# Kernel optimization log

Measured on AMD Instinct MI355X. Metric: run time of the kernel, lower is better.

## Reference

```python
import jax, jax.numpy as jnp
import numpy as np

HIDDEN = 600
INPUT_DIM = 300
BATCH = 64
SEQ = 512


def _lstm(x, W, U, b):
    """Keras-style LSTM, gate order (i, f, g, o). x: [B,T,D] -> [B,T,H]."""
    B, T, D = x.shape
    H = U.shape[0]
    xz = jnp.einsum('btd,dg->btg', x, W) + b  # precompute input projections [B,T,4H]

    def step(carry, xz_t):
        h, c = carry
        z = xz_t + h @ U  # [B,4H]
        i, f, g, o = jnp.split(z, 4, axis=-1)
        i = jax.nn.sigmoid(i)
        f = jax.nn.sigmoid(f)
        g = jnp.tanh(g)
        o = jax.nn.sigmoid(o)
        c = f * c + i * g
        h = o * jnp.tanh(c)
        return (h, c), h

    init = (jnp.zeros((B, H), x.dtype), jnp.zeros((B, H), x.dtype))
    _, hs = jax.lax.scan(step, init, jnp.swapaxes(xz, 0, 1))  # [T,B,H]
    return jnp.swapaxes(hs, 0, 1)


def _reverse_sequence(x, lengths):
    """tf.reverse_sequence along axis 1: reverse first lengths[b] steps, keep tail."""
    T = x.shape[1]
    t = jnp.arange(T)[None, :]
    L = lengths[:, None]
    idx = jnp.where(t < L, L - 1 - t, t)  # [B,T]
    return jnp.take_along_axis(x, idx[:, :, None], axis=1)


def setup_inputs() -> dict:
    key = jax.random.key(0)
    ks = jax.random.split(key, 8)
    inputs = jax.random.normal(ks[0], (BATCH, SEQ, INPUT_DIM), dtype=jnp.float32)
    lengths = jax.random.randint(ks[1], (BATCH,), 1, SEQ + 1, dtype=jnp.int32)
    s = 0.05
    Wf = jax.random.normal(ks[2], (INPUT_DIM, 4 * HIDDEN), dtype=jnp.float32) * s
    Uf = jax.random.normal(ks[3], (HIDDEN, 4 * HIDDEN), dtype=jnp.float32) * s
    bf = jnp.zeros((4 * HIDDEN,), dtype=jnp.float32)
    Wb = jax.random.normal(ks[4], (INPUT_DIM, 4 * HIDDEN), dtype=jnp.float32) * s
    Ub = jax.random.normal(ks[5], (HIDDEN, 4 * HIDDEN), dtype=jnp.float32) * s
    bb = jnp.zeros((4 * HIDDEN,), dtype=jnp.float32)
    return {"inputs": inputs, "lengths": lengths, "training": False,
            "Wf": Wf, "Uf": Uf, "bf": bf, "Wb": Wb, "Ub": Ub, "bb": bb}


def reference(inputs, lengths, training, Wf, Uf, bf, Wb, Ub, bb):
    # training=False -> Keras dropout is identity, so plain LSTMs are faithful.
    T = inputs.shape[1]
    seq_mask = (jnp.arange(T)[None, :] < lengths[:, None]).astype(inputs.dtype)  # [B,T]
    forward_outputs = _lstm(inputs, Wf, Uf, bf)
    reversed_inputs = _reverse_sequence(inputs, lengths)
    backward_outputs = _reverse_sequence(_lstm(reversed_inputs, Wb, Ub, bb), lengths)
    outputs = jnp.concatenate([forward_outputs, backward_outputs], axis=-1)  # [B,T,2H]
    outputs = outputs * seq_mask[:, :, None]
    # reduce_states=True: tf.reduce_mean over time divides by full T (not lengths)
    return jnp.mean(outputs, axis=1)
```

## Files before the change

kernel.cpp:

```cpp
#include <hip/hip_runtime.h>
#include <hip/hip_fp16.h>
#include <cmath>

typedef _Float16 f16;
typedef _Float16 half8 __attribute__((ext_vector_type(8)));
typedef float f32x4 __attribute__((ext_vector_type(4)));

#define P_WG   75
#define GRID_MAIN (2*P_WG)
#define G      12
#define RING   13

#define X16_ELEMS  (64u*512u*320u)
#define BPK_HALF   (2u*75u*2u*30u*64u*8u)
#define HBUF_F16   (2u*2u*64u*640u)
#define HBUF_WORDS (HBUF_F16/2u)
#define FLAG_WORDS 256u
#define E_OFF      96u

__global__ void lstm_prep(const float* __restrict__ x,
                          const float* __restrict__ Wf, const float* __restrict__ Uf,
                          const float* __restrict__ Wb, const float* __restrict__ Ub,
                          const int* __restrict__ len,
                          f16* __restrict__ x16h, f16* __restrict__ x16l,
                          f16* __restrict__ Bpk,
                          unsigned* __restrict__ hbw, unsigned* __restrict__ flags,
                          int* __restrict__ maxT, float* __restrict__ outp)
{
    const unsigned total = X16_ELEMS + BPK_HALF + HBUF_WORDS + FLAG_WORDS + 2u;
    for (unsigned e = blockIdx.x * blockDim.x + threadIdx.x; e < total;
         e += gridDim.x * blockDim.x) {
        if (e < X16_ELEMS) {
            unsigned k = e % 320u, r = e / 320u;
            float v = (k < 300u) ? x[r * 300u + k] : 0.0f;
            f16 hi = (f16)v;
            x16h[e] = hi;
            x16l[e] = (f16)((v - (float)hi) * 2048.0f);
        } else if (e < X16_ELEMS + BPK_HALF) {
            unsigned i = e - X16_ELEMS;
            unsigned j    = i & 7u,  r1 = i >> 3;
            unsigned lane = r1 & 63u, r2 = r1 >> 6;
            unsigned kt   = r2 % 30u, r3 = r2 / 30u;
            unsigned nt   = r3 & 1u,  r4 = r3 >> 1;
            unsigned p    = r4 % 75u, dw = r4 / 75u;
            unsigned k = kt * 32u + (lane >> 4) * 8u + j;
            unsigned n = nt * 16u + (lane & 15u);
            unsigned c = (n >> 3) * 600u + p * 8u + (n & 7u);
            float v = 0.0f;
            if (k < 300u)                    v = (dw ? Wb : Wf)[k * 2400u + c];
            else if (k >= 320u && k < 920u)  v = (dw ? Ub : Uf)[(k - 320u) * 2400u + c];
            f16 hi = (f16)v;
            unsigned base = (((((dw * 75u + p) * 2u + 0u) * 2u + nt) * 30u + kt) * 64u + lane) * 8u + j;
            Bpk[base]          = hi;
            Bpk[base + 30720u] = (f16)((v - (float)hi) * 2048.0f);
        } else if (e < X16_ELEMS + BPK_HALF + HBUF_WORDS) {
            hbw[e - X16_ELEMS - BPK_HALF] = 0u;
        } else if (e < X16_ELEMS + BPK_HALF + HBUF_WORDS + FLAG_WORDS) {
            unsigned q = e - (X16_ELEMS + BPK_HALF + HBUF_WORDS);
            unsigned q7 = q & 127u;
            flags[q] = (q7 < 75u || q7 == E_OFF) ? 0u : 0xFFFFFFFFu;
        } else {
            unsigned q = e - (X16_ELEMS + BPK_HALF + HBUF_WORDS + FLAG_WORDS);
            if (q == 0u) {
                int m = 1;
                for (int b = 0; b < 64; ++b) { int L = len[b]; m = (L > m) ? L : m; }
                *maxT = m;
            } else {
                outp[0] = 1000.0f;
            }
        }
    }
}

__global__ __launch_bounds__(256, 1)
void lstm_main(const f16* __restrict__ x16h, const f16* __restrict__ x16l,
               const f16* __restrict__ Bpk,
               f16* __restrict__ hbuf, float* __restrict__ xz,
               unsigned* flags, const int* __restrict__ maxT,
               const int* __restrict__ len,
               const float* __restrict__ bfv, const float* __restrict__ bbv,
               float* __restrict__ out)
{
    __shared__ f32x4 obox[4][4][2][64];
    __shared__ f16 hstage[64][8];
    __shared__ f16 Blds[4][10][512];

    const int tid  = threadIdx.x;
    const int wave = tid >> 6, lane = tid & 63;
    const int quad = lane >> 4, l15 = lane & 15;
    const int dir  = blockIdx.x & 1, p = blockIdx.x >> 1;
    const int pc   = p * 8;
    const int wg   = blockIdx.x;

    const int s0 = (wave < 2) ? 3 : 2;
    half8 Bh[5][2][2];
    const unsigned bpk_base = (unsigned)(dir * 75 + p) * 4u * 30u * 512u;
#pragma unroll
    for (int sp = 0; sp < 5; ++sp) {
        int kt = wave + 4 * (s0 + sp);
#pragma unroll
        for (int nt = 0; nt < 2; ++nt)
#pragma unroll
            for (int tm = 0; tm < 2; ++tm)
                Bh[sp][nt][tm] = *(const half8*)(Bpk +
                    (((((dir * 75 + p) * 2 + tm) * 2 + nt) * 30 + kt) * 64 + lane) * 8);
    }
    const float* bias = dir ? bbv : bfv;
    const float b0 = bias[((l15 >> 3)    ) * 600 + pc + (l15 & 7)];
    const float b1 = bias[((l15 >> 3) + 2) * 600 + pc + (l15 & 7)];

    int Lm[4], Lr[4];
#pragma unroll
    for (int mt = 0; mt < 4; ++mt) Lm[mt] = len[mt * 16 + l15];
    const int Lw = len[wave * 16 + l15];
#pragma unroll
    for (int r = 0; r < 4; ++r)   Lr[r]  = len[wave * 16 + quad * 4 + r];

    f16* hb0 = hbuf + dir * (2 * 64 * 640);
    unsigned* myflags = flags + dir * 128;
    float* myxz = xz + (size_t)wg * (RING * 64 * 32);
    float cst[4] = {0, 0, 0, 0}, sum[4] = {0, 0, 0, 0};
    const int T = *maxT;

    {
        f16* bl = &Blds[0][0][0];
#pragma unroll
        for (int blk = 0; blk < 4; ++blk)
            for (int i = tid; i < 640; i += 256)
                *(half8*)(bl + blk * 5120 + i * 8) =
                    *(const half8*)(Bpk + bpk_base + (unsigned)blk * 15360u + (unsigned)i * 8u);
    }
    __syncthreads();

#pragma unroll
    for (int jc = 0; jc < 3; ++jc) {
        int g = wave * 3 + jc;
        int tt = (g < 512) ? g : 511;
        unsigned arow[4];
#pragma unroll
        for (int mt = 0; mt < 4; ++mt) {
            int tx = tt;
            if (dir) tx = (tt < Lm[mt]) ? (Lm[mt] - 1 - tt) : tt;
            arow[mt] = ((unsigned)(mt * 16 + l15) * 512u + (unsigned)tx) * 320u + quad * 8;
        }
        f32x4 aH[4][2], aM[4][2];
#pragma unroll
        for (int mt = 0; mt < 4; ++mt)
#pragma unroll
            for (int nt = 0; nt < 2; ++nt) {
                aH[mt][nt] = f32x4{0.f, 0.f, 0.f, 0.f};
                aM[mt][nt] = f32x4{0.f, 0.f, 0.f, 0.f};
            }
#pragma unroll
        for (int kt = 0; kt < 10; ++kt) {
            const f16* bb = &Blds[0][0][0] + kt * 512 + lane * 8;
            half8 B00 = *(const half8*)(bb);
            half8 B01 = *(const half8*)(bb + 5120);
            half8 B10 = *(const half8*)(bb + 10240);
            half8 B11 = *(const half8*)(bb + 15360);
#pragma unroll
            for (int mt = 0; mt < 4; ++mt) {
                half8 Ah = *(const half8*)(x16h + arow[mt] + kt * 32);
                half8 Al = *(const half8*)(x16l + arow[mt] + kt * 32);
                aH[mt][0] = __builtin_amdgcn_mfma_f32_16x16x32_f16(Ah, B00, aH[mt][0], 0, 0, 0);
                aM[mt][0] = __builtin_amdgcn_mfma_f32_16x16x32_f16(Ah, B10, aM[mt][0], 0, 0, 0);
                aM[mt][0] = __builtin_amdgcn_mfma_f32_16x16x32_f16(Al, B00, aM[mt][0], 0, 0, 0);
                aH[mt][1] = __builtin_amdgcn_mfma_f32_16x16x32_f16(Ah, B01, aH[mt][1], 0, 0, 0);
                aM[mt][1] = __builtin_amdgcn_mfma_f32_16x16x32_f16(Ah, B11, aM[mt][1], 0, 0, 0);
                aM[mt][1] = __builtin_amdgcn_mfma_f32_16x16x32_f16(Al, B01, aM[mt][1], 0, 0, 0);
            }
        }
#pragma unroll
        for (int mt = 0; mt < 4; ++mt)
#pragma unroll
            for (int r = 0; r < 4; ++r) {
                unsigned rowi = (unsigned)(g * 64 + mt * 16 + quad * 4 + r) * 32u;
                myxz[rowi + l15]      = aH[mt][0][r] + aM[mt][0][r] * (1.0f / 2048.0f) + b0;
                myxz[rowi + 16 + l15] = aH[mt][1][r] + aM[mt][1][r] * (1.0f / 2048.0f) + b1;
            }
    }
    __syncthreads();

    for (int t = 0; t < T; ++t) {
        int tf = t + G;
        if (tf < T) {
            int tx = tf;
            if (dir) tx = (tf < Lw) ? (Lw - 1 - tf) : tf;
            unsigned arow = ((unsigned)(wave * 16 + l15) * 512u + (unsigned)tx) * 320u + quad * 8;
            f32x4 aH[2], aM[2];
            aH[0] = f32x4{0.f, 0.f, 0.f, 0.f}; aM[0] = f32x4{0.f, 0.f, 0.f, 0.f};
            aH[1] = f32x4{0.f, 0.f, 0.f, 0.f}; aM[1] = f32x4{0.f, 0.f, 0.f, 0.f};
#pragma unroll
            for (int kt = 0; kt < 10; ++kt) {
                const f16* bb = &Blds[0][0][0] + kt * 512 + lane * 8;
                half8 B00 = *(const half8*)(bb);
                half8 B01 = *(const half8*)(bb + 5120);
                half8 B10 = *(const half8*)(bb + 10240);
                half8 B11 = *(const half8*)(bb + 15360);
                half8 Ah = *(const half8*)(x16h + arow + kt * 32);
                half8 Al = *(const half8*)(x16l + arow + kt * 32);
                aH[0] = __builtin_amdgcn_mfma_f32_16x16x32_f16(Ah, B00, aH[0], 0, 0, 0);
                aM[0] = __builtin_amdgcn_mfma_f32_16x16x32_f16(Ah, B10, aM[0], 0, 0, 0);
                aM[0] = __builtin_amdgcn_mfma_f32_16x16x32_f16(Al, B00, aM[0], 0, 0, 0);
                aH[1] = __builtin_amdgcn_mfma_f32_16x16x32_f16(Ah, B01, aH[1], 0, 0, 0);
                aM[1] = __builtin_amdgcn_mfma_f32_16x16x32_f16(Ah, B11, aM[1], 0, 0, 0);
                aM[1] = __builtin_amdgcn_mfma_f32_16x16x32_f16(Al, B01, aM[1], 0, 0, 0);
            }
            int slot = tf % RING;
#pragma unroll
            for (int r = 0; r < 4; ++r) {
                unsigned rowi = (unsigned)(slot * 64 + wave * 16 + quad * 4 + r) * 32u;
                myxz[rowi + l15]      = aH[0][r] + aM[0][r] * (1.0f / 2048.0f) + b0;
                myxz[rowi + 16 + l15] = aH[1][r] + aM[1][r] * (1.0f / 2048.0f) + b1;
            }
        }

        float z0p[4], z1p[4];
        {
            int slot = t % RING;
            unsigned rbase = (unsigned)(slot * 64 + wave * 16 + quad * 4) * 32u;
#pragma unroll
            for (int r = 0; r < 4; ++r) {
                z0p[r] = myxz[rbase + r * 32 + l15];
                z1p[r] = myxz[rbase + r * 32 + 16 + l15];
            }
        }

        const f16* hcur = hb0 + (t & 1) * (64 * 640);
        f16*       hnxt = hb0 + ((t + 1) & 1) * (64 * 640);

        if (t > 0) {
            const unsigned tgt = (unsigned)t;
            if (wave == 0) {
                const unsigned long long* f8 = (const unsigned long long*)myflags;
                for (;;) {
                    unsigned long long v = ~0ull;
                    if (lane < 38)
                        v = __hip_atomic_load(&f8[lane], __ATOMIC_RELAXED, __HIP_MEMORY_SCOPE_AGENT);
                    bool bad = ((unsigned)v < tgt) || ((unsigned)(v >> 32) < tgt);
                    if (!__any(bad)) break;
                    __builtin_amdgcn_s_sleep(1);
                }
            }
            __syncthreads();
        }

        f32x4 accH[4][2], accM[4][2];
#pragma unroll
        for (int mt = 0; mt < 4; ++mt)
#pragma unroll
            for (int nt = 0; nt < 2; ++nt) {
                accH[mt][nt] = f32x4{0.f, 0.f, 0.f, 0.f};
                accM[mt][nt] = f32x4{0.f, 0.f, 0.f, 0.f};
            }

        unsigned long long pre[3][8];
        const f16* hq = hcur + quad * 8;
#define HLOAD(W, SP)                                                                     \
        { const int kt_ = wave + 4 * (s0 + (SP));                                        \
          const f16* hp_ = hq + (kt_ * 32 - 320);                                        \
          _Pragma("unroll")                                                              \
          for (int mt_ = 0; mt_ < 4; ++mt_) {                                            \
              const unsigned long long* q_ =                                             \
                  (const unsigned long long*)(hp_ + (unsigned)(mt_ * 16 + l15) * 640u);  \
              pre[W][mt_ * 2]     = __hip_atomic_load(q_,     __ATOMIC_RELAXED,          \
                                                      __HIP_MEMORY_SCOPE_AGENT);         \
              pre[W][mt_ * 2 + 1] = __hip_atomic_load(q_ + 1, __ATOMIC_RELAXED,          \
                                                      __HIP_MEMORY_SCOPE_AGENT);         \
          } }

        HLOAD(0, 0)
        HLOAD(1, 1)
        HLOAD(2, 2)
#pragma unroll
        for (int sp = 0; sp < 5; ++sp) {
#pragma unroll
            for (int mt = 0; mt < 4; ++mt) {
                union { unsigned long long u[2]; half8 h; } xu;
                xu.u[0] = pre[sp % 3][mt * 2];
                xu.u[1] = pre[sp % 3][mt * 2 + 1];
                half8 Ah = xu.h;
                accH[mt][0] = __builtin_amdgcn_mfma_f32_16x16x32_f16(Ah, Bh[sp][0][0], accH[mt][0], 0, 0, 0);
                accM[mt][0] = __builtin_amdgcn_mfma_f32_16x16x32_f16(Ah, Bh[sp][0][1], accM[mt][0], 0, 0, 0);
                accH[mt][1] = __builtin_amdgcn_mfma_f32_16x16x32_f16(Ah, Bh[sp][1][0], accH[mt][1], 0, 0, 0);
                accM[mt][1] = __builtin_amdgcn_mfma_f32_16x16x32_f16(Ah, Bh[sp][1][1], accM[mt][1], 0, 0, 0);
            }
            if (sp == 0) HLOAD(0, 3)
            if (sp == 1) HLOAD(1, 4)
        }
#undef HLOAD

        __syncthreads();
#pragma unroll
        for (int mt = 0; mt < 4; ++mt)
#pragma unroll
            for (int nt = 0; nt < 2; ++nt)
                obox[wave][mt][nt][lane] = accH[mt][nt] + accM[mt][nt] * (1.0f / 2048.0f);
        __syncthreads();
        f32x4 z0 = obox[0][wave][0][lane] + obox[1][wave][0][lane]
                 + obox[2][wave][0][lane] + obox[3][wave][0][lane];
        f32x4 z1 = obox[0][wave][1][lane] + obox[1][wave][1][lane]
                 + obox[2][wave][1][lane] + obox[3][wave][1][lane];
        z0 += f32x4{z0p[0], z0p[1], z0p[2], z0p[3]};
        z1 += f32x4{z1p[0], z1p[1], z1p[2], z1p[3]};

#pragma unroll
        for (int r = 0; r < 4; ++r) {
            float zi = z0[r], zg = z1[r];
            float zf = __shfl_xor(z0[r], 8, 64);
            float zo = __shfl_xor(z1[r], 8, 64);
            if (l15 < 8) {
                float ig = 1.0f / (1.0f + __expf(-zi));
                float fg = 1.0f / (1.0f + __expf(-zf));
                float gg = tanhf(zg);
                float og = 1.0f / (1.0f + __expf(-zo));
                float c  = fg * cst[r] + ig * gg;
                cst[r] = c;
                float h = og * tanhf(c);
                if (t < Lr[r]) sum[r] += h;
                hstage[wave * 16 + quad * 4 + r][l15] = (f16)h;
            }
        }
        __syncthreads();
        if (tid < 128) {
            int rr = tid >> 1, hf = tid & 1;
            unsigned long long v = *(const unsigned long long*)&hstage[rr][hf * 4];
            __hip_atomic_store(
                (unsigned long long*)(hnxt + (unsigned)rr * 640u + pc + hf * 4),
                v, __ATOMIC_RELAXED, __HIP_MEMORY_SCOPE_AGENT);
        }
        __syncthreads();
        if (tid == 0)
            __hip_atomic_store(myflags + p, (unsigned)(t + 1),
                               __ATOMIC_RELAXED, __HIP_MEMORY_SCOPE_AGENT);
    }

    if (l15 < 8) {
#pragma unroll
        for (int r = 0; r < 4; ++r)
            out[(wave * 16 + quad * 4 + r) * 1200 + dir * 600 + pc + l15] =
                sum[r] * (1.0f / 512.0f);
    }
}

extern "C" void kernel_launch(void* const* d_in, const int* in_sizes, int n_in,
                              void* d_out, int out_size, void* d_ws, size_t ws_size,
                              hipStream_t stream) {
    const float* x   = (const float*)d_in[0];
    const int*   len = (const int*)  d_in[1];
    const float* Wf  = (const float*)d_in[3];
    const float* Uf  = (const float*)d_in[4];
    const float* bfv = (const float*)d_in[5];
    const float* Wb  = (const float*)d_in[6];
    const float* Ub  = (const float*)d_in[7];
    const float* bbv = (const float*)d_in[8];
    float* outp = (float*)d_out;

    char* w = (char*)d_ws;
    f16*      x16hp = (f16*)w;
    f16*      x16lp = (f16*)(w + 20971520);
    f16*      bpkp  = (f16*)(w + 41943040);
    f16*      hbufp = (f16*)(w + 60375040);
    float*    xzp   = (float*)(w + 60702720);
    unsigned* flagp = (unsigned*)(w + 76677120);
    int*      maxtp = (int*)(w + 76678144);

    hipLaunchKernelGGL(lstm_prep, dim3(1024), dim3(256), 0, stream,
                       x, Wf, Uf, Wb, Ub, len,
                       x16hp, x16lp, bpkp, (unsigned*)hbufp, flagp, maxtp, outp);

    hipLaunchKernelGGL(lstm_main, dim3(GRID_MAIN), dim3(256), 0, stream,
                       x16hp, x16lp, bpkp, hbufp, xzp, flagp, maxtp, len, bfv, bbv, outp);
}
```

Baseline: 4.954 ms.

## Interleave forward and backward directions within each workgroup, halving grid

The grid shrinks from 150 to 75 workgroups, and each workgroup now processes both LSTM directions in alternation at every timestep. Recurrent weights are reloaded from global memory per step instead of staying resident in registers. Both directions' input-projection tiles are kept in LDS. The likely intent is to overlap one direction's flag wait and latency with the other's compute, at the cost of serialising both directions on one CU. It also adds per-step weight reload traffic and doubles LDS use.

Result: slower. 9.751 ms (+96.9%).

```diff
diff --git a/kernel.cpp b/kernel.cpp
--- a/kernel.cpp
+++ b/kernel.cpp
@@ -7,7 +7,7 @@
 typedef float f32x4 __attribute__((ext_vector_type(4)));
 
 #define P_WG   75
-#define GRID_MAIN (2*P_WG)
+#define GRID_MAIN P_WG
 #define G      12
 #define RING   13
 
@@ -58,7 +58,7 @@
         } else if (e < X16_ELEMS + BPK_HALF + HBUF_WORDS + FLAG_WORDS) {
             unsigned q = e - (X16_ELEMS + BPK_HALF + HBUF_WORDS);
             unsigned q7 = q & 127u;
-            flags[q] = (q7 < 75u || q7 == E_OFF) ? 0u : 0xFFFFFFFFu;
+            flags[q] = (q7 < 75u) ? 0u : 0xFFFFFFFFu;
         } else {
             unsigned q = e - (X16_ELEMS + BPK_HALF + HBUF_WORDS + FLAG_WORDS);
             if (q == 0u) {
@@ -83,31 +83,29 @@
 {
     __shared__ f32x4 obox[4][4][2][64];
     __shared__ f16 hstage[64][8];
-    __shared__ f16 Blds[4][10][512];
+    __shared__ f16 Blds[2][4][10][512];
 
     const int tid  = threadIdx.x;
     const int wave = tid >> 6, lane = tid & 63;
     const int quad = lane >> 4, l15 = lane & 15;
-    const int dir  = blockIdx.x & 1, p = blockIdx.x >> 1;
+    const int p    = blockIdx.x;
     const int pc   = p * 8;
-    const int wg   = blockIdx.x;
 
     const int s0 = (wave < 2) ? 3 : 2;
-    half8 Bh[5][2][2];
-    const unsigned bpk_base = (unsigned)(dir * 75 + p) * 4u * 30u * 512u;
-#pragma unroll
-    for (int sp = 0; sp < 5; ++sp) {
-        int kt = wave + 4 * (s0 + sp);
-#pragma unroll
-        for (int nt = 0; nt < 2; ++nt)
-#pragma unroll
-            for (int tm = 0; tm < 2; ++tm)
-                Bh[sp][nt][tm] = *(const half8*)(Bpk +
-                    (((((dir * 75 + p) * 2 + tm) * 2 + nt) * 30 + kt) * 64 + lane) * 8);
-    }
-    const float* bias = dir ? bbv : bfv;
-    const float b0 = bias[((l15 >> 3)    ) * 600 + pc + (l15 & 7)];
-    const float b1 = bias[((l15 >> 3) + 2) * 600 + pc + (l15 & 7)];
+
+    const unsigned bb_base[2] = { (unsigned)(0 * 75 + p) * 4u * 30u * 512u,
+                                  (unsigned)(1 * 75 + p) * 4u * 30u * 512u };
+    f16* hb[2]      = { hbuf, hbuf + (2 * 64 * 640) };
+    unsigned* fl[2] = { flags, flags + 128 };
+    float* mx[2]    = { xz + (size_t)(p * 2 + 0) * (RING * 64 * 32),
+                        xz + (size_t)(p * 2 + 1) * (RING * 64 * 32) };
+    float b0a[2], b1a[2];
+    {
+        const int c0 = ((l15 >> 3)) * 600 + pc + (l15 & 7);
+        const int c1 = ((l15 >> 3) + 2) * 600 + pc + (l15 & 7);
+        b0a[0] = bfv[c0]; b1a[0] = bfv[c1];
+        b0a[1] = bbv[c0]; b1a[1] = bbv[c1];
+    }
 
     int Lm[4], Lr[4];
 #pragma unroll
@@ -116,231 +114,250 @@
 #pragma unroll
     for (int r = 0; r < 4; ++r)   Lr[r]  = len[wave * 16 + quad * 4 + r];
 
-    f16* hb0 = hbuf + dir * (2 * 64 * 640);
-    unsigned* myflags = flags + dir * 128;
-    float* myxz = xz + (size_t)wg * (RING * 64 * 32);
-    float cst[4] = {0, 0, 0, 0}, sum[4] = {0, 0, 0, 0};
+    float cst[2][4] = {{0,0,0,0},{0,0,0,0}}, sum[2][4] = {{0,0,0,0},{0,0,0,0}};
     const int T = *maxT;
 
-    {
-        f16* bl = &Blds[0][0][0];
+#pragma unroll
+    for (int dd = 0; dd < 2; ++dd) {
+        f16* bl = &Blds[dd][0][0][0];
 #pragma unroll
         for (int blk = 0; blk < 4; ++blk)
             for (int i = tid; i < 640; i += 256)
                 *(half8*)(bl + blk * 5120 + i * 8) =
-                    *(const half8*)(Bpk + bpk_base + (unsigned)blk * 15360u + (unsigned)i * 8u);
+                    *(const half8*)(Bpk + bb_base[dd] + (unsigned)blk * 15360u + (unsigned)i * 8u);
     }
     __syncthreads();
 
 #pragma unroll
-    for (int jc = 0; jc < 3; ++jc) {
-        int g = wave * 3 + jc;
-        int tt = (g < 512) ? g : 511;
-        unsigned arow[4];
-#pragma unroll
-        for (int mt = 0; mt < 4; ++mt) {
-            int tx = tt;
-            if (dir) tx = (tt < Lm[mt]) ? (Lm[mt] - 1 - tt) : tt;
-            arow[mt] = ((unsigned)(mt * 16 + l15) * 512u + (unsigned)tx) * 320u + quad * 8;
-        }
-        f32x4 aH[4][2], aM[4][2];
-#pragma unroll
-        for (int mt = 0; mt < 4; ++mt)
-#pragma unroll
-            for (int nt = 0; nt < 2; ++nt) {
-                aH[mt][nt] = f32x4{0.f, 0.f, 0.f, 0.f};
-                aM[mt][nt] = f32x4{0.f, 0.f, 0.f, 0.f};
-            }
-#pragma unroll
-        for (int kt = 0; kt < 10; ++kt) {
-            const f16* bb = &Blds[0][0][0] + kt * 512 + lane * 8;
-            half8 B00 = *(const half8*)(bb);
-            half8 B01 = *(const half8*)(bb + 5120);
-            half8 B10 = *(const half8*)(bb + 10240);
-            half8 B11 = *(const half8*)(bb + 15360);
+    for (int dd = 0; dd < 2; ++dd) {
+#pragma unroll
+        for (int jc = 0; jc < 3; ++jc) {
+            int g = wave * 3 + jc;
+            int tt = (g < 512) ? g : 511;
+            unsigned arow[4];
 #pragma unroll
             for (int mt = 0; mt < 4; ++mt) {
-                half8 Ah = *(const half8*)(x16h + arow[mt] + kt * 32);
-                half8 Al = *(const half8*)(x16l + arow[mt] + kt * 32);
-                aH[mt][0] = __builtin_amdgcn_mfma_f32_16x16x32_f16(Ah, B00, aH[mt][0], 0, 0, 0);
-                aM[mt][0] = __builtin_amdgcn_mfma_f32_16x16x32_f16(Ah, B10, aM[mt][0], 0, 0, 0);
-                aM[mt][0] = __builtin_amdgcn_mfma_f32_16x16x32_f16(Al, B00, aM[mt][0], 0, 0, 0);
-                aH[mt][1] = __builtin_amdgcn_mfma_f32_16x16x32_f16(Ah, B01, aH[mt][1], 0, 0, 0);
-                aM[mt][1] = __builtin_amdgcn_mfma_f32_16x16x32_f16(Ah, B11, aM[mt][1], 0, 0, 0);
-                aM[mt][1] = __builtin_amdgcn_mfma_f32_16x16x32_f16(Al, B01, aM[mt][1], 0, 0, 0);
-            }
-        }
-#pragma unroll
-        for (int mt = 0; mt < 4; ++mt)
-#pragma unroll
-            for (int r = 0; r < 4; ++r) {
-                unsigned rowi = (unsigned)(g * 64 + mt * 16 + quad * 4 + r) * 32u;
-                myxz[rowi + l15]      = aH[mt][0][r] + aM[mt][0][r] * (1.0f / 2048.0f) + b0;
-                myxz[rowi + 16 + l15] = aH[mt][1][r] + aM[mt][1][r] * (1.0f / 2048.0f) + b1;
-            }
-    }
-    __syncthreads();
-
-    for (int t = 0; t < T; ++t) {
-        int tf = t + G;
-        if (tf < T) {
-            int tx = tf;
-            if (dir) tx = (tf < Lw) ? (Lw - 1 - tf) : tf;
-            unsigned arow = ((unsigned)(wave * 16 + l15) * 512u + (unsigned)tx) * 320u + quad * 8;
-            f32x4 aH[2], aM[2];
-            aH[0] = f32x4{0.f, 0.f, 0.f, 0.f}; aM[0] = f32x4{0.f, 0.f, 0.f, 0.f};
-            aH[1] = f32x4{0.f, 0.f, 0.f, 0.f}; aM[1] = f32x4{0.f, 0.f, 0.f, 0.f};
+                int tx = tt;
+                if (dd) tx = (tt < Lm[mt]) ? (Lm[mt] - 1 - tt) : tt;
+                arow[mt] = ((unsigned)(mt * 16 + l15) * 512u + (unsigned)tx) * 320u + quad * 8;
+            }
+            f32x4 aH[4][2], aM[4][2];
+#pragma unroll
+            for (int mt = 0; mt < 4; ++mt)
+#pragma unroll
+                for (int nt = 0; nt < 2; ++nt) {
+                    aH[mt][nt] = f32x4{0.f, 0.f, 0.f, 0.f};
+                    aM[mt][nt] = f32x4{0.f, 0.f, 0.f, 0.f};
+                }
 #pragma unroll
             for (int kt = 0; kt < 10; ++kt) {
-                const f16* bb = &Blds[0][0][0] + kt * 512 + lane * 8;
+                const f16* bb = &Blds[dd][0][0][0] + kt * 512 + lane * 8;
                 half8 B00 = *(const half8*)(bb);
                 half8 B01 = *(const half8*)(bb + 5120);
                 half8 B10 = *(const half8*)(bb + 10240);
                 half8 B11 = *(const half8*)(bb + 15360);
-                half8 Ah = *(const half8*)(x16h + arow + kt * 32);
-                half8 Al = *(const half8*)(x16l + arow + kt * 32);
-                aH[0] = __builtin_amdgcn_mfma_f32_16x16x32_f16(Ah, B00, aH[0], 0, 0, 0);
-                aM[0] = __builtin_amdgcn_mfma_f32_16x16x32_f16(Ah, B10, aM[0], 0, 0, 0);
-                aM[0] = __builtin_amdgcn_mfma_f32_16x16x32_f16(Al, B00, aM[0], 0, 0, 0);
-                aH[1] = __builtin_amdgcn_mfma_f32_16x16x32_f16(Ah, B01, aH[1], 0, 0, 0);
-                aM[1] = __builtin_amdgcn_mfma_f32_16x16x32_f16(Ah, B11, aM[1], 0, 0, 0);
-                aM[1] = __builtin_amdgcn_mfma_f32_16x16x32_f16(Al, B01, aM[1], 0, 0, 0);
-            }
-            int slot = tf % RING;
+#pragma unroll
+                for (int mt = 0; mt < 4; ++mt) {
+                    half8 Ah = *(const half8*)(x16h + arow[mt] + kt * 32);
+                    half8 Al = *(const half8*)(x16l + arow[mt] + kt * 32);
+                    aH[mt][0] = __builtin_amdgcn_mfma_f32_16x16x32_f16(Ah, B00, aH[mt][0], 0, 0, 0);
+                    aM[mt][0] = __builtin_amdgcn_mfma_f32_16x16x32_f16(Ah, B10, aM[mt][0], 0, 0, 0);
+                    aM[mt][0] = __builtin_amdgcn_mfma_f32_16x16x32_f16(Al, B00, aM[mt][0], 0, 0, 0);
+                    aH[mt][1] = __builtin_amdgcn_mfma_f32_16x16x32_f16(Ah, B01, aH[mt][1], 0, 0, 0);
+                    aM[mt][1] = __builtin_amdgcn_mfma_f32_16x16x32_f16(Ah, B11, aM[mt][1], 0, 0, 0);
+                    aM[mt][1] = __builtin_amdgcn_mfma_f32_16x16x32_f16(Al, B01, aM[mt][1], 0, 0, 0);
+                }
+            }
+#pragma unroll
+            for (int mt = 0; mt < 4; ++mt)
+#pragma unroll
+                for (int r = 0; r < 4; ++r) {
+                    unsigned rowi = (unsigned)(g * 64 + mt * 16 + quad * 4 + r) * 32u;
+                    mx[dd][rowi + l15]      = aH[mt][0][r] + aM[mt][0][r] * (1.0f / 2048.0f) + b0a[dd];
+                    mx[dd][rowi + 16 + l15] = aH[mt][1][r] + aM[mt][1][r] * (1.0f / 2048.0f) + b1a[dd];
+                }
+        }
+    }
+    __syncthreads();
+
+    for (int t = 0; t < T; ++t) {
+#pragma unroll
+        for (int dd = 0; dd < 2; ++dd) {
+            half8 Bh[5][2][2];
+#pragma unroll
+            for (int sp = 0; sp < 5; ++sp) {
+                int kt = wave + 4 * (s0 + sp);
+#pragma unroll
+                for (int nt = 0; nt < 2; ++nt)
+#pragma unroll
+                    for (int tm = 0; tm < 2; ++tm)
+                        Bh[sp][nt][tm] = *(const half8*)(Bpk + bb_base[dd] +
+                            ((unsigned)(tm * 2 + nt) * 30u + (unsigned)kt) * 512u + lane * 8);
+            }
+
+            float z0p[4], z1p[4];
+            {
+                int slot = t % RING;
+                unsigned rbase = (unsigned)(slot * 64 + wave * 16 + quad * 4) * 32u;
+#pragma unroll
+                for (int r = 0; r < 4; ++r) {
+                    z0p[r] = mx[dd][rbase + r * 32 + l15];
+                    z1p[r] = mx[dd][rbase + r * 32 + 16 + l15];
+                }
+            }
+
+            const f16* hcur = hb[dd] + (t & 1) * (64 * 640);
+            f16*       hnxt = hb[dd] + ((t + 1) & 1) * (64 * 640);
+            unsigned*  myflags = fl[dd];
+
+            if (t > 0) {
+                const unsigned tgt = (unsigned)t;
+                if (wave == 0) {
+                    const unsigned long long* f8 = (const unsigned long long*)myflags;
+                    for (;;) {
+                        unsigned long long v = ~0ull;
+                        if (lane < 38)
+                            v = __hip_atomic_load(&f8[lane], __ATOMIC_RELAXED, __HIP_MEMORY_SCOPE_AGENT);
+                        bool bad = ((unsigned)v < tgt) || ((unsigned)(v >> 32) < tgt);
+                        if (!__any(bad)) break;
+                        __builtin_amdgcn_s_sleep(1);
+                    }
+                }
+                __syncthreads();
+            }
+
+            f32x4 accH[4][2], accM[4][2];
+#pragma unroll
+            for (int mt = 0; mt < 4; ++mt)
+#pragma unroll
+                for (int nt = 0; nt < 2; ++nt) {
+                    accH[mt][nt] = f32x4{0.f, 0.f, 0.f, 0.f};
+                    accM[mt][nt] = f32x4{0.f, 0.f, 0.f, 0.f};
+                }
+
+            unsigned long long pre[3][8];
+            const f16* hq = hcur + quad * 8;
+#define HLOAD(W, SP)                                                                     \
+            { const int kt_ = wave + 4 * (s0 + (SP));                                    \
+              const f16* hp_ = hq + (kt_ * 32 - 320);                                    \
+              _Pragma("unroll")                                                          \
+              for (int mt_ = 0; mt_ < 4; ++mt_) {                                        \
+                  const unsigned long long* q_ =                                         \
+                      (const unsigned long long*)(hp_ + (unsigned)(mt_ * 16 + l15) * 640u); \
+                  pre[W][mt_ * 2]     = __hip_atomic_load(q_,     __ATOMIC_RELAXED,      \
+                                                          __HIP_MEMORY_SCOPE_AGENT);     \
+                  pre[W][mt_ * 2 + 1] = __hip_atomic_load(q_ + 1, __ATOMIC_RELAXED,      \
+                                                          __HIP_MEMORY_SCOPE_AGENT);     \
+              } }
+
+            HLOAD(0, 0)
+            HLOAD(1, 1)
+            HLOAD(2, 2)
+#pragma unroll
+            for (int sp = 0; sp < 5; ++sp) {
+#pragma unroll
+                for (int mt = 0; mt < 4; ++mt) {
+                    union { unsigned long long u[2]; half8 h; } xu;
+                    xu.u[0] = pre[sp % 3][mt * 2];
+                    xu.u[1] = pre[sp % 3][mt * 2 + 1];
+                    half8 Ah = xu.h;
+                    accH[mt][0] = __builtin_amdgcn_mfma_f32_16x16x32_f16(Ah, Bh[sp][0][0], accH[mt][0], 0, 0, 0);
+                    accM[mt][0] = __builtin_amdgcn_mfma_f32_16x16x32_f16(Ah, Bh[sp][0][1], accM[mt][0], 0, 0, 0);
+                    accH[mt][1] = __builtin_amdgcn_mfma_f32_16x16x32_f16(Ah, Bh[sp][1][0], accH[mt][1], 0, 0, 0);
+                    accM[mt][1] = __builtin_amdgcn_mfma_f32_16x16x32_f16(Ah, Bh[sp][1][1], accM[mt][1], 0, 0, 0);
+                }
+                if (sp == 0) HLOAD(0, 3)
+                if (sp == 1) HLOAD(1, 4)
+            }
+#undef HLOAD
+
+            __syncthreads();
+#pragma unroll
+            for (int mt = 0; mt < 4; ++mt)
+#pragma unroll
+                for (int nt = 0; nt < 2; ++nt)
+                    obox[wave][mt][nt][lane] = accH[mt][nt] + accM[mt][nt] * (1.0f / 2048.0f);
+            __syncthreads();
+            f32x4 z0 = obox[0][wave][0][lane] + obox[1][wave][0][lane]
+                     + obox[2][wave][0][lane] + obox[3][wave][0][lane];
+            f32x4 z1 = obox[0][wave][1][lane] + obox[1][wave][1][lane]
+                     + obox[2][wave][1][lane] + obox[3][wave][1][lane];
+            z0 += f32x4{z0p[0], z0p[1], z0p[2], z0p[3]};
+            z1 += f32x4{z1p[0], z1p[1], z1p[2], z1p[3]};
+
 #pragma unroll
             for (int r = 0; r < 4; ++r) {
-                unsigned rowi = (unsigned)(slot * 64 + wave * 16 + quad * 4 + r) * 32u;
-                myxz[rowi + l15]      = aH[0][r] + aM[0][r] * (1.0f / 2048.0f) + b0;
-                myxz[rowi + 16 + l15] = aH[1][r] + aM[1][r] * (1.0f / 2048.0f) + b1;
+                float zi = z0[r], zg = z1[r];
+                float zf = __shfl_xor(z0[r], 8, 64);
+                float zo = __shfl_xor(z1[r], 8, 64);
+                if (l15 < 8) {
+                    float ig = 1.0f / (1.0f + __expf(-zi));
+                    float fg = 1.0f / (1.0f + __expf(-zf));
+                    float gg = tanhf(zg);
+                    float og = 1.0f / (1.0f + __expf(-zo));
+                    float c  = fg * cst[dd][r] + ig * gg;
+                    cst[dd][r] = c;
+                    float h = og * tanhf(c);
+                    if (t < Lr[r]) sum[dd][r] += h;
+                    hstage[wave * 16 + quad * 4 + r][l15] = (f16)h;
+                }
+            }
+            __syncthreads();
+            if (tid < 128) {
+                int rr = tid >> 1, hf = tid & 1;
+                unsigned long long v = *(const unsigned long long*)&hstage[rr][hf * 4];
+                __hip_atomic_store(
+                    (unsigned long long*)(hnxt + (unsigned)rr * 640u + pc + hf * 4),
+                    v, __ATOMIC_RELAXED, __HIP_MEMORY_SCOPE_AGENT);
+            }
+            __syncthreads();
+            if (tid == 0)
+                __hip_atomic_store(myflags + p, (unsigned)(t + 1),
+                                   __ATOMIC_RELAXED, __HIP_MEMORY_SCOPE_AGENT);
+
+            int tf = t + G;
+            if (tf < T) {
+                int tx = tf;
+                if (dd) tx = (tf < Lw) ? (Lw - 1 - tf) : tf;
+                unsigned arow = ((unsigned)(wave * 16 + l15) * 512u + (unsigned)tx) * 320u + quad * 8;
+                f32x4 aH[2], aM[2];
+                aH[0] = f32x4{0.f, 0.f, 0.f, 0.f}; aM[0] = f32x4{0.f, 0.f, 0.f, 0.f};
+                aH[1] = f32x4{0.f, 0.f, 0.f, 0.f}; aM[1] = f32x4{0.f, 0.f, 0.f, 0.f};
+#pragma unroll
+                for (int kt = 0; kt < 10; ++kt) {
+                    const f16* bb = &Blds[dd][0][0][0] + kt * 512 + lane * 8;
+                    half8 B00 = *(const half8*)(bb);
+                    half8 B01 = *(const half8*)(bb + 5120);
+                    half8 B10 = *(const half8*)(bb + 10240);
+                    half8 B11 = *(const half8*)(bb + 15360);
+                    half8 Ah = *(const half8*)(x16h + arow + kt * 32);
+                    half8 Al = *(const half8*)(x16l + arow + kt * 32);
+                    aH[0] = __builtin_amdgcn_mfma_f32_16x16x32_f16(Ah, B00, aH[0], 0, 0, 0);
+                    aM[0] = __builtin_amdgcn_mfma_f32_16x16x32_f16(Ah, B10, aM[0], 0, 0, 0);
+                    aM[0] = __builtin_amdgcn_mfma_f32_16x16x32_f16(Al, B00, aM[0], 0, 0, 0);
+                    aH[1] = __builtin_amdgcn_mfma_f32_16x16x32_f16(Ah, B01, aH[1], 0, 0, 0);
+                    aM[1] = __builtin_amdgcn_mfma_f32_16x16x32_f16(Ah, B11, aM[1], 0, 0, 0);
+                    aM[1] = __builtin_amdgcn_mfma_f32_16x16x32_f16(Al, B01, aM[1], 0, 0, 0);
+                }
+                int slot = tf % RING;
+#pragma unroll
+                for (int r = 0; r < 4; ++r) {
+                    unsigned rowi = (unsigned)(slot * 64 + wave * 16 + quad * 4 + r) * 32u;
+                    mx[dd][rowi + l15]      = aH[0][r] + aM[0][r] * (1.0f / 2048.0f) + b0a[dd];
+                    mx[dd][rowi + 16 + l15] = aH[1][r] + aM[1][r] * (1.0f / 2048.0f) + b1a[dd];
+                }
             }
         }
-
-        float z0p[4], z1p[4];
-        {
-            int slot = t % RING;
-            unsigned rbase = (unsigned)(slot * 64 + wave * 16 + quad * 4) * 32u;
-#pragma unroll
-            for (int r = 0; r < 4; ++r) {
-                z0p[r] = myxz[rbase + r * 32 + l15];
-                z1p[r] = myxz[rbase + r * 32 + 16 + l15];
-            }
+    }
+
+#pragma unroll
+    for (int dd = 0; dd < 2; ++dd)
+        if (l15 < 8) {
+#pragma unroll
+            for (int r = 0; r < 4; ++r)
+                out[(wave * 16 + quad * 4 + r) * 1200 + dd * 600 + pc + l15] =
+                    sum[dd][r] * (1.0f / 512.0f);
         }
-
-        const f16* hcur = hb0 + (t & 1) * (64 * 640);
-        f16*       hnxt = hb0 + ((t + 1) & 1) * (64 * 640);
-
-        if (t > 0) {
-            const unsigned tgt = (unsigned)t;
-            if (wave == 0) {
-                const unsigned long long* f8 = (const unsigned long long*)myflags;
-                for (;;) {
-                    unsigned long long v = ~0ull;
-                    if (lane < 38)
-                        v = __hip_atomic_load(&f8[lane], __ATOMIC_RELAXED, __HIP_MEMORY_SCOPE_AGENT);
-                    bool bad = ((unsigned)v < tgt) || ((unsigned)(v >> 32) < tgt);
-                    if (!__any(bad)) break;
-                    __builtin_amdgcn_s_sleep(1);
-                }
-            }
-            __syncthreads();
-        }
-
-        f32x4 accH[4][2], accM[4][2];
-#pragma unroll
-        for (int mt = 0; mt < 4; ++mt)
-#pragma unroll
-            for (int nt = 0; nt < 2; ++nt) {
-                accH[mt][nt] = f32x4{0.f, 0.f, 0.f, 0.f};
-                accM[mt][nt] = f32x4{0.f, 0.f, 0.f, 0.f};
-            }
-
-        unsigned long long pre[3][8];
-        const f16* hq = hcur + quad * 8;
-#define HLOAD(W, SP)                                                                     \
-        { const int kt_ = wave + 4 * (s0 + (SP));                                        \
-          const f16* hp_ = hq + (kt_ * 32 - 320);                                        \
-          _Pragma("unroll")                                                              \
-          for (int mt_ = 0; mt_ < 4; ++mt_) {                                            \
-              const unsigned long long* q_ =                                             \
-                  (const unsigned long long*)(hp_ + (unsigned)(mt_ * 16 + l15) * 640u);  \
-              pre[W][mt_ * 2]     = __hip_atomic_load(q_,     __ATOMIC_RELAXED,          \
-                                                      __HIP_MEMORY_SCOPE_AGENT);         \
-              pre[W][mt_ * 2 + 1] = __hip_atomic_load(q_ + 1, __ATOMIC_RELAXED,          \
-                                                      __HIP_MEMORY_SCOPE_AGENT);         \
-          } }
-
-        HLOAD(0, 0)
-        HLOAD(1, 1)
-        HLOAD(2, 2)
-#pragma unroll
-        for (int sp = 0; sp < 5; ++sp) {
-#pragma unroll
-            for (int mt = 0; mt < 4; ++mt) {
-                union { unsigned long long u[2]; half8 h; } xu;
-                xu.u[0] = pre[sp % 3][mt * 2];
-                xu.u[1] = pre[sp % 3][mt * 2 + 1];
-                half8 Ah = xu.h;
-                accH[mt][0] = __builtin_amdgcn_mfma_f32_16x16x32_f16(Ah, Bh[sp][0][0], accH[mt][0], 0, 0, 0);
-                accM[mt][0] = __builtin_amdgcn_mfma_f32_16x16x32_f16(Ah, Bh[sp][0][1], accM[mt][0], 0, 0, 0);
-                accH[mt][1] = __builtin_amdgcn_mfma_f32_16x16x32_f16(Ah, Bh[sp][1][0], accH[mt][1], 0, 0, 0);
-                accM[mt][1] = __builtin_amdgcn_mfma_f32_16x16x32_f16(Ah, Bh[sp][1][1], accM[mt][1], 0, 0, 0);
-            }
-            if (sp == 0) HLOAD(0, 3)
-            if (sp == 1) HLOAD(1, 4)
-        }
-#undef HLOAD
-
-        __syncthreads();
-#pragma unroll
-        for (int mt = 0; mt < 4; ++mt)
-#pragma unroll
-            for (int nt = 0; nt < 2; ++nt)
-                obox[wave][mt][nt][lane] = accH[mt][nt] + accM[mt][nt] * (1.0f / 2048.0f);
-        __syncthreads();
-        f32x4 z0 = obox[0][wave][0][lane] + obox[1][wave][0][lane]
-                 + obox[2][wave][0][lane] + obox[3][wave][0][lane];
-        f32x4 z1 = obox[0][wave][1][lane] + obox[1][wave][1][lane]
-                 + obox[2][wave][1][lane] + obox[3][wave][1][lane];
-        z0 += f32x4{z0p[0], z0p[1], z0p[2], z0p[3]};
-        z1 += f32x4{z1p[0], z1p[1], z1p[2], z1p[3]};
-
-#pragma unroll
-        for (int r = 0; r < 4; ++r) {
-            float zi = z0[r], zg = z1[r];
-            float zf = __shfl_xor(z0[r], 8, 64);
-            float zo = __shfl_xor(z1[r], 8, 64);
-            if (l15 < 8) {
-                float ig = 1.0f / (1.0f + __expf(-zi));
-                float fg = 1.0f / (1.0f + __expf(-zf));
-                float gg = tanhf(zg);
-                float og = 1.0f / (1.0f + __expf(-zo));
-                float c  = fg * cst[r] + ig * gg;
-                cst[r] = c;
-                float h = og * tanhf(c);
-                if (t < Lr[r]) sum[r] += h;
-                hstage[wave * 16 + quad * 4 + r][l15] = (f16)h;
-            }
-        }
-        __syncthreads();
-        if (tid < 128) {
-            int rr = tid >> 1, hf = tid & 1;
-            unsigned long long v = *(const unsigned long long*)&hstage[rr][hf * 4];
-            __hip_atomic_store(
-                (unsigned long long*)(hnxt + (unsigned)rr * 640u + pc + hf * 4),
-                v, __ATOMIC_RELAXED, __HIP_MEMORY_SCOPE_AGENT);
-        }
-        __syncthreads();
-        if (tid == 0)
-            __hip_atomic_store(myflags + p, (unsigned)(t + 1),
-                               __ATOMIC_RELAXED, __HIP_MEMORY_SCOPE_AGENT);
-    }
-
-    if (l15 < 8) {
-#pragma unroll
-        for (int r = 0; r < 4; ++r)
-            out[(wave * 16 + quad * 4 + r) * 1200 + dir * 600 + pc + l15] =
-                sum[r] * (1.0f / 512.0f);
-    }
 }
 
 extern "C" void kernel_launch(void* const* d_in, const int* in_sizes, int n_in,
```

## Move future input projection after recurrent matmul, stage U weights in LDS, fast activations

Applied to the files above, without the earlier changes.

The input-projection MFMA for step t+G now runs after the recurrent h@U matmul, with its x loads issued before the flag spin so they overlap the wait. The recurrent U weights move from registers into a larger LDS buffer, and the sleep in the spin-wait loop is dropped. Sigmoid and tanh switch to rcp/exp-based approximations. The aim is to hide the projection work and global load latency behind the synchronisation wait, at the cost of extra LDS reads every step, more LDS use, and slightly lower activation accuracy.

After: 4.703 ms. 5.1% less time.

```diff
diff --git a/kernel.cpp b/kernel.cpp
--- a/kernel.cpp
+++ b/kernel.cpp
@@ -16,7 +16,6 @@
 #define HBUF_F16   (2u*2u*64u*640u)
 #define HBUF_WORDS (HBUF_F16/2u)
 #define FLAG_WORDS 256u
-#define E_OFF      96u
 
 __global__ void lstm_prep(const float* __restrict__ x,
                           const float* __restrict__ Wf, const float* __restrict__ Uf,
@@ -58,7 +57,7 @@
         } else if (e < X16_ELEMS + BPK_HALF + HBUF_WORDS + FLAG_WORDS) {
             unsigned q = e - (X16_ELEMS + BPK_HALF + HBUF_WORDS);
             unsigned q7 = q & 127u;
-            flags[q] = (q7 < 75u || q7 == E_OFF) ? 0u : 0xFFFFFFFFu;
+            flags[q] = (q7 < 75u) ? 0u : 0xFFFFFFFFu;
         } else {
             unsigned q = e - (X16_ELEMS + BPK_HALF + HBUF_WORDS + FLAG_WORDS);
             if (q == 0u) {
@@ -70,6 +69,15 @@
             }
         }
     }
+}
+
+__device__ __forceinline__ float fsigm(float x) {
+    return __builtin_amdgcn_rcpf(1.0f + __expf(-x));
+}
+__device__ __forceinline__ float ftanh(float x) {
+    x = fminf(fmaxf(x, -15.0f), 15.0f);
+    float e = __expf(2.0f * x);
+    return (e - 1.0f) * __builtin_amdgcn_rcpf(e + 1.0f);
 }
 
 __global__ __launch_bounds__(256, 1)
@@ -83,7 +91,8 @@
 {
     __shared__ f32x4 obox[4][4][2][64];
     __shared__ f16 hstage[64][8];
-    __shared__ f16 Blds[4][10][512];
+    __shared__ f16 Bldsx[4][10][512];
+    __shared__ f16 Bldsh[4][20][512];
 
     const int tid  = threadIdx.x;
     const int wave = tid >> 6, lane = tid & 63;
@@ -93,18 +102,8 @@
     const int wg   = blockIdx.x;
 
     const int s0 = (wave < 2) ? 3 : 2;
-    half8 Bh[5][2][2];
     const unsigned bpk_base = (unsigned)(dir * 75 + p) * 4u * 30u * 512u;
-#pragma unroll
-    for (int sp = 0; sp < 5; ++sp) {
-        int kt = wave + 4 * (s0 + sp);
-#pragma unroll
-        for (int nt = 0; nt < 2; ++nt)
-#pragma unroll
-            for (int tm = 0; tm < 2; ++tm)
-                Bh[sp][nt][tm] = *(const half8*)(Bpk +
-                    (((((dir * 75 + p) * 2 + tm) * 2 + nt) * 30 + kt) * 64 + lane) * 8);
-    }
+
     const float* bias = dir ? bbv : bfv;
     const float b0 = bias[((l15 >> 3)    ) * 600 + pc + (l15 & 7)];
     const float b1 = bias[((l15 >> 3) + 2) * 600 + pc + (l15 & 7)];
@@ -123,12 +122,17 @@
     const int T = *maxT;
 
     {
-        f16* bl = &Blds[0][0][0];
-#pragma unroll
-        for (int blk = 0; blk < 4; ++blk)
+#pragma unroll
+        for (int blk = 0; blk < 4; ++blk) {
+            f16* blx = &Bldsx[blk][0][0];
             for (int i = tid; i < 640; i += 256)
-                *(half8*)(bl + blk * 5120 + i * 8) =
+                *(half8*)(blx + i * 8) =
                     *(const half8*)(Bpk + bpk_base + (unsigned)blk * 15360u + (unsigned)i * 8u);
+            f16* blh = &Bldsh[blk][0][0];
+            for (int i = tid; i < 1280; i += 256)
+                *(half8*)(blh + i * 8) =
+                    *(const half8*)(Bpk + bpk_base + (unsigned)blk * 15360u + 5120u + (unsigned)i * 8u);
+        }
     }
     __syncthreads();
 
@@ -153,7 +157,7 @@
             }
 #pragma unroll
         for (int kt = 0; kt < 10; ++kt) {
-            const f16* bb = &Blds[0][0][0] + kt * 512 + lane * 8;
+            const f16* bb = &Bldsx[0][0][0] + kt * 512 + lane * 8;
             half8 B00 = *(const half8*)(bb);
             half8 B01 = *(const half8*)(bb + 5120);
             half8 B10 = *(const half8*)(bb + 10240);
@@ -183,37 +187,19 @@
 
     for (int t = 0; t < T; ++t) {
         int tf = t + G;
-        if (tf < T) {
-            int tx = tf;
-            if (dir) tx = (tf < Lw) ? (Lw - 1 - tf) : tf;
+        int tq = (tf < T) ? tf : (T - 1);
+        half8 axh[10], axl[10];
+        {
+            int tx = tq;
+            if (dir) tx = (tq < Lw) ? (Lw - 1 - tq) : tq;
             unsigned arow = ((unsigned)(wave * 16 + l15) * 512u + (unsigned)tx) * 320u + quad * 8;
-            f32x4 aH[2], aM[2];
-            aH[0] = f32x4{0.f, 0.f, 0.f, 0.f}; aM[0] = f32x4{0.f, 0.f, 0.f, 0.f};
-            aH[1] = f32x4{0.f, 0.f, 0.f, 0.f}; aM[1] = f32x4{0.f, 0.f, 0.f, 0.f};
 #pragma unroll
             for (int kt = 0; kt < 10; ++kt) {
-                const f16* bb = &Blds[0][0][0] + kt * 512 + lane * 8;
-                half8 B00 = *(const half8*)(bb);
-                half8 B01 = *(const half8*)(bb + 5120);
-                half8 B10 = *(const half8*)(bb + 10240);
-                half8 B11 = *(const half8*)(bb + 15360);
-                half8 Ah = *(const half8*)(x16h + arow + kt * 32);
-                half8 Al = *(const half8*)(x16l + arow + kt * 32);
-                aH[0] = __builtin_amdgcn_mfma_f32_16x16x32_f16(Ah, B00, aH[0], 0, 0, 0);
-                aM[0] = __builtin_amdgcn_mfma_f32_16x16x32_f16(Ah, B10, aM[0], 0, 0, 0);
-                aM[0] = __builtin_amdgcn_mfma_f32_16x16x32_f16(Al, B00, aM[0], 0, 0, 0);
-                aH[1] = __builtin_amdgcn_mfma_f32_16x16x32_f16(Ah, B01, aH[1], 0, 0, 0);
-                aM[1] = __builtin_amdgcn_mfma_f32_16x16x32_f16(Ah, B11, aM[1], 0, 0, 0);
-                aM[1] = __builtin_amdgcn_mfma_f32_16x16x32_f16(Al, B01, aM[1], 0, 0, 0);
-            }
-            int slot = tf % RING;
-#pragma unroll
-            for (int r = 0; r < 4; ++r) {
-                unsigned rowi = (unsigned)(slot * 64 + wave * 16 + quad * 4 + r) * 32u;
-                myxz[rowi + l15]      = aH[0][r] + aM[0][r] * (1.0f / 2048.0f) + b0;
-                myxz[rowi + 16 + l15] = aH[1][r] + aM[1][r] * (1.0f / 2048.0f) + b1;
-            }
-        }
+                axh[kt] = *(const half8*)(x16h + arow + kt * 32);
+                axl[kt] = *(const half8*)(x16l + arow + kt * 32);
+            }
+        }
+        __builtin_amdgcn_sched_barrier(0);
 
         float z0p[4], z1p[4];
         {
@@ -239,7 +225,6 @@
                         v = __hip_atomic_load(&f8[lane], __ATOMIC_RELAXED, __HIP_MEMORY_SCOPE_AGENT);
                     bool bad = ((unsigned)v < tgt) || ((unsigned)(v >> 32) < tgt);
                     if (!__any(bad)) break;
-                    __builtin_amdgcn_s_sleep(1);
                 }
             }
             __syncthreads();
@@ -274,21 +259,56 @@
         HLOAD(2, 2)
 #pragma unroll
         for (int sp = 0; sp < 5; ++sp) {
+            const int kt = wave + 4 * (s0 + sp);
+            const f16* bh = &Bldsh[0][0][0] + (kt - 10) * 512 + lane * 8;
+            half8 Bc00 = *(const half8*)(bh);
+            half8 Bc01 = *(const half8*)(bh + 10240);
+            half8 Bc10 = *(const half8*)(bh + 20480);
+            half8 Bc11 = *(const half8*)(bh + 30720);
 #pragma unroll
             for (int mt = 0; mt < 4; ++mt) {
                 union { unsigned long long u[2]; half8 h; } xu;
                 xu.u[0] = pre[sp % 3][mt * 2];
                 xu.u[1] = pre[sp % 3][mt * 2 + 1];
                 half8 Ah = xu.h;
-                accH[mt][0] = __builtin_amdgcn_mfma_f32_16x16x32_f16(Ah, Bh[sp][0][0], accH[mt][0], 0, 0, 0);
-                accM[mt][0] = __builtin_amdgcn_mfma_f32_16x16x32_f16(Ah, Bh[sp][0][1], accM[mt][0], 0, 0, 0);
-                accH[mt][1] = __builtin_amdgcn_mfma_f32_16x16x32_f16(Ah, Bh[sp][1][0], accH[mt][1], 0, 0, 0);
-                accM[mt][1] = __builtin_amdgcn_mfma_f32_16x16x32_f16(Ah, Bh[sp][1][1], accM[mt][1], 0, 0, 0);
+                accH[mt][0] = __builtin_amdgcn_mfma_f32_16x16x32_f16(Ah, Bc00, accH[mt][0], 0, 0, 0);
+                accM[mt][0] = __builtin_amdgcn_mfma_f32_16x16x32_f16(Ah, Bc10, accM[mt][0], 0, 0, 0);
+                accH[mt][1] = __builtin_amdgcn_mfma_f32_16x16x32_f16(Ah, Bc01, accH[mt][1], 0, 0, 0);
+                accM[mt][1] = __builtin_amdgcn_mfma_f32_16x16x32_f16(Ah, Bc11, accM[mt][1], 0, 0, 0);
             }
             if (sp == 0) HLOAD(0, 3)
             if (sp == 1) HLOAD(1, 4)
         }
 #undef HLOAD
+
+        {
+            f32x4 aH[2], aM[2];
+            aH[0] = f32x4{0.f, 0.f, 0.f, 0.f}; aM[0] = f32x4{0.f, 0.f, 0.f, 0.f};
+            aH[1] = f32x4{0.f, 0.f, 0.f, 0.f}; aM[1] = f32x4{0.f, 0.f, 0.f, 0.f};
+#pragma unroll
+            for (int kt = 0; kt < 10; ++kt) {
+                const f16* bb = &Bldsx[0][0][0] + kt * 512 + lane * 8;
+                half8 B00 = *(const half8*)(bb);
+                half8 B01 = *(const half8*)(bb + 5120);
+                half8 B10 = *(const half8*)(bb + 10240);
+                half8 B11 = *(const half8*)(bb + 15360);
+                aH[0] = __builtin_amdgcn_mfma_f32_16x16x32_f16(axh[kt], B00, aH[0], 0, 0, 0);
+                aM[0] = __builtin_amdgcn_mfma_f32_16x16x32_f16(axh[kt], B10, aM[0], 0, 0, 0);
+                aM[0] = __builtin_amdgcn_mfma_f32_16x16x32_f16(axl[kt], B00, aM[0], 0, 0, 0);
+                aH[1] = __builtin_amdgcn_mfma_f32_16x16x32_f16(axh[kt], B01, aH[1], 0, 0, 0);
+                aM[1] = __builtin_amdgcn_mfma_f32_16x16x32_f16(axh[kt], B11, aM[1], 0, 0, 0);
+                aM[1] = __builtin_amdgcn_mfma_f32_16x16x32_f16(axl[kt], B01, aM[1], 0, 0, 0);
+            }
+            if (tf < T) {
+                int slot = tf % RING;
+#pragma unroll
+                for (int r = 0; r < 4; ++r) {
+                    unsigned rowi = (unsigned)(slot * 64 + wave * 16 + quad * 4 + r) * 32u;
+                    myxz[rowi + l15]      = aH[0][r] + aM[0][r] * (1.0f / 2048.0f) + b0;
+                    myxz[rowi + 16 + l15] = aH[1][r] + aM[1][r] * (1.0f / 2048.0f) + b1;
+                }
+            }
+        }
 
         __syncthreads();
 #pragma unroll
@@ -310,13 +330,13 @@
             float zf = __shfl_xor(z0[r], 8, 64);
             float zo = __shfl_xor(z1[r], 8, 64);
             if (l15 < 8) {
-                float ig = 1.0f / (1.0f + __expf(-zi));
-                float fg = 1.0f / (1.0f + __expf(-zf));
-                float gg = tanhf(zg);
-                float og = 1.0f / (1.0f + __expf(-zo));
+                float ig = fsigm(zi);
+                float fg = fsigm(zf);
+                float gg = ftanh(zg);
+                float og = fsigm(zo);
                 float c  = fg * cst[r] + ig * gg;
                 cst[r] = c;
-                float h = og * tanhf(c);
+                float h = og * ftanh(c);
                 if (t < Lr[r]) sum[r] += h;
                 hstage[wave * 16 + quad * 4 + r][l15] = (f16)h;
             }
```
